# Kernel optimization log

Measured on AMD Instinct MI355X. Metric: run time of the kernel, lower is better.

Reference implementation:

```python
import jax, jax.numpy as jnp
import numpy as np

SEGMENT_LENGTHS = [1024, 2048, 4096]
DILATION_RATES = [1, 2, 4]


def setup_inputs() -> dict:
    key = jax.random.key(0)
    k1, k2, k3 = jax.random.split(key, 3)
    n = sum(SEGMENT_LENGTHS)  # 7168
    shape = (1, n, 8, 64)  # (b, n, h, d)
    q = jax.random.normal(k1, shape, dtype=jnp.float32)
    k = jax.random.normal(k2, shape, dtype=jnp.float32)
    v = jax.random.normal(k3, shape, dtype=jnp.float32)
    return {"q": q, "k": k, "v": v}


def _attend(q_seg, k_kv, v_kv):
    # q_seg: [b, q_len, h, d]; k_kv/v_kv: [b, k_len, h, d]
    d = q_seg.shape[-1]
    scale = 1.0 / jnp.sqrt(jnp.asarray(d, q_seg.dtype))
    scores = jnp.einsum("bqhd,bkhd->bhqk", q_seg, k_kv) * scale
    w = jax.nn.softmax(scores, axis=-1)
    return jnp.einsum("bhqk,bkhd->bqhd", w, v_kv)


def reference(q, k, v):
    # Single-device dilated attention (ring_size == 1, is_causal=False).
    n = q.shape[1]
    output = jnp.zeros_like(q)
    seg_start = 0
    for seg_len, dilation in zip(SEGMENT_LENGTHS, DILATION_RATES):
        if seg_start >= n:
            break
        seg_end = min(seg_start + seg_len, n)
        q_seg = q[:, seg_start:seg_end]
        if dilation > 1:
            k_d = k[:, ::dilation]
            v_d = v[:, ::dilation]
        else:
            k_d, v_d = k, v
        out_seg = _attend(q_seg, k_d, v_d)
        output = output.at[:, seg_start:seg_end].set(out_seg)
        seg_start = seg_end
    return output
```

## Files before the change

### kernel.cpp

```cpp
#include <hip/hip_runtime.h>

#define VB0 3670016L
#define VB1 7340032L
#define VB2 9175040L
#define PO_OFF 5046272L
#define PL_OFF (PO_OFF + 512L * 128 * 64)

typedef short bvec8 __attribute__((ext_vector_type(8)));
typedef float fvec16 __attribute__((ext_vector_type(16)));

static __device__ __forceinline__ short f2bf(float f) {
  unsigned u = __float_as_uint(f);
  u = u + 0x7fffu + ((u >> 16) & 1u);
  return (short)(u >> 16);
}

#if defined(__has_builtin)
#if __has_builtin(__builtin_amdgcn_cvt_pk_bf16_f32)
#define HAVE_CVTPK 1
#endif
#if __has_builtin(__builtin_amdgcn_permlane32_swap)
#define HAVE_PLSWAP 1
#endif
#endif

static __device__ __forceinline__ unsigned pk2(float a, float b) {
#ifdef HAVE_CVTPK
  auto r = __builtin_amdgcn_cvt_pk_bf16_f32(a, b);
  unsigned u; __builtin_memcpy(&u, &r, 4);
  return u;
#else
  unsigned ua = (__float_as_uint(a) + 0x8000u) >> 16;
  unsigned ub = (__float_as_uint(b) + 0x8000u) & 0xffff0000u;
  return ua | ub;
#endif
}
static __device__ __forceinline__ void async16(const short* g, short* l) {
  __builtin_amdgcn_global_load_lds((const __attribute__((address_space(1))) unsigned*)(void*)g,
                                   (__attribute__((address_space(3))) unsigned*)(void*)l, 16, 0, 0);
}

__global__ __launch_bounds__(256) void pack_all(const float* __restrict__ k,
                                                const float* __restrict__ v,
                                                short* __restrict__ W) {
  __shared__ float tl[64][65];
  int b = blockIdx.x, t = threadIdx.x;
  if (b < 896) {
    int h = b / 112, tile = b % 112, i0 = tile * 64;
    int r = t >> 2, c = t & 3;
    const float* src = k + ((long)(i0 + r) * 8 + h) * 64 + c * 16;
    short* dst = W + ((long)h * 7168 + i0 + r) * 64 + c * 16;
    union { unsigned u[8]; bvec8 v[2]; } tw;
#pragma unroll
    for (int q4 = 0; q4 < 4; q4++) {
      float4 x = *(const float4*)(src + q4 * 4);
      tw.u[q4 * 2 + 0] = pk2(x.x, x.y);
      tw.u[q4 * 2 + 1] = pk2(x.z, x.w);
    }
    *(bvec8*)dst = tw.v[0];
    *(bvec8*)(dst + 8) = tw.v[1];
  } else {
    int b2 = b - 896;
    int h, tile, dil, L; long base;
    if (b2 < 896)       { L = 7168; dil = 1; h = b2 / 112; tile = b2 % 112; base = VB0; }
    else if (b2 < 1344) { int bb = b2 - 896;  L = 3584; dil = 2; h = bb / 56; tile = bb % 56; base = VB1; }
    else                { int bb = b2 - 1344; L = 1792; dil = 4; h = bb / 28; tile = bb % 28; base = VB2; }
    int i0 = tile * 64;
    int row = t >> 2, c = t & 3;
    const float* src = v + ((long)(i0 + row) * dil * 8 + h) * 64;
#pragma unroll
    for (int cc = 0; cc < 4; cc++) {
      int d0 = c * 16 + cc * 4;
      float4 x = *(const float4*)(src + d0);
      tl[row][d0 + 0] = x.x; tl[row][d0 + 1] = x.y;
      tl[row][d0 + 2] = x.z; tl[row][d0 + 3] = x.w;
    }
    __syncthreads();
    int d = t >> 2, part = t & 3;
    union { unsigned u[8]; bvec8 v[2]; } tw;
#pragma unroll
    for (int u2 = 0; u2 < 8; u2++)
      tw.u[u2] = pk2(tl[part * 16 + 2 * u2][d], tl[part * 16 + 2 * u2 + 1][d]);
    short* dst = W + base + ((long)h * 64 + d) * L + i0 + part * 16;
    *(bvec8*)dst = tw.v[0];
    *(bvec8*)(dst + 8) = tw.v[1];
  }
}

__global__ __launch_bounds__(256, 3) void attn_kern(const float* __restrict__ q,
                                                    const short* __restrict__ W,
                                                    float* __restrict__ out,
                                                    float* __restrict__ PO,
                                                    float* __restrict__ PL) {
  int b = blockIdx.x;
  int h, q0, dil, kt0, L; long vbo;
  if (b < 256)      { int sp = b & 3; h = (b >> 2) & 7; int qt = b >> 5;
                      q0 = qt * 128;        dil = 1; L = 7168; vbo = VB0; kt0 = sp * 28; }
  else if (b < 512) { int i = b - 256; int sp = i & 1; h = (i >> 1) & 7; int qt = i >> 4;
                      q0 = 1024 + qt * 128; dil = 2; L = 3584; vbo = VB1; kt0 = sp * 28; }
  else              { int i = b - 512; h = i & 7; int qt = i >> 3;
                      q0 = 3072 + qt * 128; dil = 4; L = 1792; vbo = VB2; kt0 = 0; }
  const short* kb = W + (long)h * 7168 * 64;
  const short* vt = W + vbo + (long)h * 64 * L;
  const int dil64 = dil * 64;

  __shared__ __attribute__((aligned(16))) short sK[2][4096];
  __shared__ __attribute__((aligned(16))) short sV[2][4096];
  short* sKf = &sK[0][0];
  short* sVf = &sV[0][0];

  int t = threadIdx.x, lane = t & 63, w = t >> 6;
  int ln = lane & 31, hb = lane >> 5;

  bvec8 qb[4];
  {
    const float* qp = q + ((long)(q0 + w * 32 + ln) * 8 + h) * 64 + 8 * hb;
    const float qs = 0.125f * 1.44269504088896f;
#pragma unroll
    for (int ks = 0; ks < 4; ks++) {
      union { unsigned u[4]; bvec8 v; } qu;
#pragma unroll
      for (int jj = 0; jj < 4; jj++)
        qu.u[jj] = pk2(qs * qp[ks * 16 + 2 * jj], qs * qp[ks * 16 + 2 * jj + 1]);
      qb[ks] = qu.v;
    }
  }

  bvec8 onesf;
#pragma unroll
  for (int j = 0; j < 8; j++) onesf[j] = (short)0x3F80;

  int srow = lane >> 3, sch = (lane & 7) ^ srow;
  auto stage = [&](int keybase, int buf) {
#pragma unroll
    for (int r2 = 0; r2 < 2; r2++) {
      int row = (w * 2 + r2) * 8 + srow;
      const short* gpk = kb + (long)(keybase + row) * dil64 + sch * 8;
      async16(gpk, sKf + (long)buf * 4096 + (w * 2 + r2) * 512);
      const short* gpv = vt + (long)row * L + keybase + sch * 8;
      async16(gpv, sVf + (long)buf * 4096 + (w * 2 + r2) * 512);
    }
  };

  stage(kt0 * 64, 0);

  int koff[8];
#pragma unroll
  for (int ks = 0; ks < 4; ks++)
#pragma unroll
    for (int mb = 0; mb < 2; mb++)
      koff[ks * 2 + mb] = (mb * 32 + ln) * 64 + (((2 * ks + hb) ^ (ln & 7)) * 8);

  fvec16 Oa[2], La;
#pragma unroll
  for (int i = 0; i < 16; i++) { Oa[0][i] = 0.f; Oa[1][i] = 0.f; La[i] = 0.f; }

  for (int it = 0; it < 28; it++) {
    int buf = it & 1;
    int key0 = (kt0 + it) * 64;
    __syncthreads();

    if (it < 27) stage(key0 + 64, buf ^ 1);

    fvec16 Sa[2];
#pragma unroll
    for (int i = 0; i < 16; i++) { Sa[0][i] = 0.f; Sa[1][i] = 0.f; }
    const short* sb = sKf + (long)buf * 4096;
    __builtin_amdgcn_s_setprio(1);
#pragma unroll
    for (int ks = 0; ks < 4; ks++)
#pragma unroll
      for (int mb = 0; mb < 2; mb++) {
        bvec8 kf = *(const bvec8*)(sb + koff[ks * 2 + mb]);
        Sa[mb] = __builtin_amdgcn_mfma_f32_32x32x16_bf16(kf, qb[ks], Sa[mb], 0, 0, 0);
      }
    __builtin_amdgcn_s_setprio(0);

    const short* vbuf = sVf + (long)buf * 4096;
    bvec8 vf[8];
#pragma unroll
    for (int ks = 0; ks < 4; ks++)
#pragma unroll
      for (int mb = 0; mb < 2; mb++)
        vf[mb * 4 + ks] = *(const bvec8*)(vbuf + koff[ks * 2 + mb]);

#pragma unroll
    for (int ks2 = 0; ks2 < 4; ks2++) {
      int mb = ks2 >> 1, r0i = (ks2 & 1) * 8;
      float p[8];
#pragma unroll
      for (int u = 0; u < 8; u++)
        p[u] = __builtin_amdgcn_exp2f(Sa[mb][r0i + u]);
      unsigned da0 = pk2(p[0], p[1]), da1 = pk2(p[2], p[3]);
      unsigned db0 = pk2(p[4], p[5]), db1 = pk2(p[6], p[7]);
      union { unsigned u[4]; bvec8 v; } fu;
#ifdef HAVE_PLSWAP
      {
        auto rr0 = __builtin_amdgcn_permlane32_swap((int)da0, (int)db0, false, false);
        auto rr1 = __builtin_amdgcn_permlane32_swap((int)da1, (int)db1, false, false);
        __builtin_memcpy(&fu.u[0], &rr0, 4);
        __builtin_memcpy(&fu.u[2], (const char*)&rr0 + 4, 4);
        __builtin_memcpy(&fu.u[1], &rr1, 4);
        __builtin_memcpy(&fu.u[3], (const char*)&rr1 + 4, 4);
      }
#else
      unsigned s0 = hb ? da0 : db0, s1 = hb ? da1 : db1;
      unsigned x0 = __shfl_xor(s0, 32), x1 = __shfl_xor(s1, 32);
      fu.u[0] = hb ? x0 : da0;  fu.u[1] = hb ? x1 : da1;
      fu.u[2] = hb ? db0 : x0;  fu.u[3] = hb ? db1 : x1;
#endif
      __builtin_amdgcn_s_setprio(1);
      Oa[0] = __builtin_amdgcn_mfma_f32_32x32x16_bf16(vf[ks2], fu.v, Oa[0], 0, 0, 0);
      Oa[1] = __builtin_amdgcn_mfma_f32_32x32x16_bf16(vf[4 + ks2], fu.v, Oa[1], 0, 0, 0);
      La    = __builtin_amdgcn_mfma_f32_32x32x16_bf16(onesf, fu.v, La, 0, 0, 0);
      __builtin_amdgcn_s_setprio(0);
    }
  }

  float lf = La[0];
  int wl = w * 32 + ln;
  if (b < 512) {
    float* po = PO + ((long)b * 128 + wl) * 64;
#pragma unroll
    for (int mb2 = 0; mb2 < 2; mb2++)
#pragma unroll
      for (int r2 = 0; r2 < 4; r2++) {
        float4 x = { Oa[mb2][r2 * 4 + 0], Oa[mb2][r2 * 4 + 1],
                     Oa[mb2][r2 * 4 + 2], Oa[mb2][r2 * 4 + 3] };
        *(float4*)(po + mb2 * 32 + r2 * 8 + hb * 4) = x;
      }
    if (hb == 0) PL[(long)b * 128 + wl] = lf;
  } else {
    float inv = 1.f / lf;
    float* op = out + ((long)(q0 + wl) * 8 + h) * 64;
#pragma unroll
    for (int mb2 = 0; mb2 < 2; mb2++)
#pragma unroll
      for (int r2 = 0; r2 < 4; r2++) {
        float4 x = { Oa[mb2][r2 * 4 + 0] * inv, Oa[mb2][r2 * 4 + 1] * inv,
                     Oa[mb2][r2 * 4 + 2] * inv, Oa[mb2][r2 * 4 + 3] * inv };
        *(float4*)(op + mb2 * 32 + r2 * 8 + hb * 4) = x;
      }
  }
}

__global__ __launch_bounds__(256) void combine_kern(const float* __restrict__ PO,
                                                    const float* __restrict__ PL,
                                                    float* __restrict__ out) {
  int g = blockIdx.x, t = threadIdx.x;
  int base_b, nsp, q0, h;
  if (g < 64) { int qt = g >> 3; h = g & 7; base_b = qt * 32 + h * 4; nsp = 4; q0 = qt * 128; }
  else { int gi = g - 64; int qt = gi >> 3; h = gi & 7; base_b = 256 + qt * 16 + h * 2; nsp = 2; q0 = 1024 + qt * 128; }
  int r = t >> 1, ch = (t & 1) * 32;
  float lt = 0.f;
  for (int sp = 0; sp < nsp; sp++) lt += PL[(long)(base_b + sp) * 128 + r];
  float inv = 1.f / lt;
  float4 acc[8];
#pragma unroll
  for (int j = 0; j < 8; j++) { acc[j].x = 0.f; acc[j].y = 0.f; acc[j].z = 0.f; acc[j].w = 0.f; }
  for (int sp = 0; sp < nsp; sp++) {
    const float4* pb = (const float4*)(PO + ((long)(base_b + sp) * 128 + r) * 64 + ch);
#pragma unroll
    for (int j = 0; j < 8; j++) {
      float4 x = pb[j];
      acc[j].x += x.x; acc[j].y += x.y; acc[j].z += x.z; acc[j].w += x.w;
    }
  }
  float4* op = (float4*)(out + ((long)(q0 + r) * 8 + h) * 64 + ch);
#pragma unroll
  for (int j = 0; j < 8; j++) {
    float4 x = { acc[j].x * inv, acc[j].y * inv, acc[j].z * inv, acc[j].w * inv };
    op[j] = x;
  }
}

extern "C" void kernel_launch(void* const* d_in, const int* in_sizes, int n_in,
                              void* d_out, int out_size, void* d_ws, size_t ws_size,
                              hipStream_t stream) {
  const float* q = (const float*)d_in[0];
  const float* k = (const float*)d_in[1];
  const float* v = (const float*)d_in[2];
  float* out = (float*)d_out;
  short* W = (short*)d_ws;
  float* PO = (float*)d_ws + PO_OFF;
  float* PL = (float*)d_ws + PL_OFF;

  pack_all<<<2464, 256, 0, stream>>>(k, v, W);
  attn_kern<<<768, 256, 0, stream>>>(q, W, out, PO, PL);
  combine_kern<<<192, 256, 0, stream>>>(PO, PL, out);
}
```

Measured before the change: 158.2 us.

## Triple-buffer K/V tiles with explicit vmcnt waits and incremental pointers

Shared-memory staging for K and V grows from two buffers to three, so loads run two tiles ahead. The full __syncthreads is replaced by a partial s_waitcnt vmcnt plus s_barrier, which lets the newest tile's loads stay in flight. Global addresses are now precomputed and advanced by a fixed stride, and the V fragment reads from LDS are moved ahead of the QK MFMAs. LDS use per block rises by half, which may limit the 3-blocks-per-CU occupancy target, and the hand-written vmcnt counts must match the number of async loads issued.

```diff
diff --git a/kernel.cpp b/kernel.cpp
--- a/kernel.cpp
+++ b/kernel.cpp
@@ -104,8 +104,8 @@
   const short* vt = W + vbo + (long)h * 64 * L;
   const int dil64 = dil * 64;
 
-  __shared__ __attribute__((aligned(16))) short sK[2][4096];
-  __shared__ __attribute__((aligned(16))) short sV[2][4096];
+  __shared__ __attribute__((aligned(16))) short sK[3][4096];
+  __shared__ __attribute__((aligned(16))) short sV[3][4096];
   short* sKf = &sK[0][0];
   short* sVf = &sV[0][0];
 
@@ -131,18 +131,27 @@
   for (int j = 0; j < 8; j++) onesf[j] = (short)0x3F80;
 
   int srow = lane >> 3, sch = (lane & 7) ^ srow;
-  auto stage = [&](int keybase, int buf) {
-#pragma unroll
-    for (int r2 = 0; r2 < 2; r2++) {
-      int row = (w * 2 + r2) * 8 + srow;
-      const short* gpk = kb + (long)(keybase + row) * dil64 + sch * 8;
-      async16(gpk, sKf + (long)buf * 4096 + (w * 2 + r2) * 512);
-      const short* gpv = vt + (long)row * L + keybase + sch * 8;
-      async16(gpv, sVf + (long)buf * 4096 + (w * 2 + r2) * 512);
-    }
+  const long kstep = 64L * dil64;
+  const short* gk0; const short* gk1; const short* gv0; const short* gv1;
+  {
+    int row0 = (w * 2 + 0) * 8 + srow, row1 = (w * 2 + 1) * 8 + srow;
+    long kb0 = (long)kt0 * 64;
+    gk0 = kb + (kb0 + row0) * dil64 + sch * 8;
+    gk1 = kb + (kb0 + row1) * dil64 + sch * 8;
+    gv0 = vt + (long)row0 * L + kb0 + sch * 8;
+    gv1 = vt + (long)row1 * L + kb0 + sch * 8;
+  }
+  const int ldoff = w * 2 * 512;
+  auto stage = [&](int bo) {
+    async16(gk0, sKf + bo + ldoff);
+    async16(gv0, sVf + bo + ldoff);
+    async16(gk1, sKf + bo + ldoff + 512);
+    async16(gv1, sVf + bo + ldoff + 512);
+    gk0 += kstep; gk1 += kstep; gv0 += 64; gv1 += 64;
   };
 
-  stage(kt0 * 64, 0);
+  stage(0);
+  stage(4096);
 
   int koff[8];
 #pragma unroll
@@ -155,17 +164,30 @@
 #pragma unroll
   for (int i = 0; i < 16; i++) { Oa[0][i] = 0.f; Oa[1][i] = 0.f; La[i] = 0.f; }
 
+  int bo = 0;
+  int bs = 8192;
   for (int it = 0; it < 28; it++) {
-    int buf = it & 1;
-    int key0 = (kt0 + it) * 64;
-    __syncthreads();
-
-    if (it < 27) stage(key0 + 64, buf ^ 1);
+    if (it < 27) asm volatile("s_waitcnt vmcnt(4)" ::: "memory");
+    else         asm volatile("s_waitcnt vmcnt(0)" ::: "memory");
+    __builtin_amdgcn_s_barrier();
+    asm volatile("" ::: "memory");
+
+    if (it < 26) { stage(bs); bs = (bs == 8192) ? 0 : bs + 4096; }
+
+    const short* sb   = sKf + bo;
+    const short* vbuf = sVf + bo;
+    bo = (bo == 8192) ? 0 : bo + 4096;
+
+    bvec8 vf[8];
+#pragma unroll
+    for (int ks = 0; ks < 4; ks++)
+#pragma unroll
+      for (int mb = 0; mb < 2; mb++)
+        vf[mb * 4 + ks] = *(const bvec8*)(vbuf + koff[ks * 2 + mb]);
 
     fvec16 Sa[2];
 #pragma unroll
     for (int i = 0; i < 16; i++) { Sa[0][i] = 0.f; Sa[1][i] = 0.f; }
-    const short* sb = sKf + (long)buf * 4096;
     __builtin_amdgcn_s_setprio(1);
 #pragma unroll
     for (int ks = 0; ks < 4; ks++)
@@ -175,14 +197,6 @@
         Sa[mb] = __builtin_amdgcn_mfma_f32_32x32x16_bf16(kf, qb[ks], Sa[mb], 0, 0, 0);
       }
     __builtin_amdgcn_s_setprio(0);
-
-    const short* vbuf = sVf + (long)buf * 4096;
-    bvec8 vf[8];
-#pragma unroll
-    for (int ks = 0; ks < 4; ks++)
-#pragma unroll
-      for (int mb = 0; mb < 2; mb++)
-        vf[mb * 4 + ks] = *(const bvec8*)(vbuf + koff[ks * 2 + mb]);
 
 #pragma unroll
     for (int ks2 = 0; ks2 < 4; ks2++) {
```

Result: no change. 159.5 us (+0.8%).
